# Kernel tuning notes

Hardware: AMD Instinct MI355X
Metric: run time of the kernel (lower is better)

## Reference

```python
import jax, jax.numpy as jnp
import numpy as np
import math

B, C, H, W = 16, 256, 96, 96
S = 3  # num_stages
OUT_C = 64


def _pos_encoding(c, h, w):
    # Faithful vectorization of generate_fixed_cosine_positional_encoding.
    pos_y = jnp.linspace(0.0, 1.0, h)
    pos_x = jnp.linspace(0.0, 1.0, w)
    py, px = jnp.meshgrid(pos_y, pos_x, indexing='ij')  # [H, W]
    i_vals = np.arange(0, c // 2, 2)                    # loop indices i
    freqs = jnp.exp(jnp.asarray(i_vals, jnp.float32) * -(math.log(10000.0) / (c // 2)))  # div_term[i//2]
    sin_part = jnp.sin(px[None] * freqs[:, None, None]) + jnp.sin(py[None] * freqs[:, None, None])
    cos_part = jnp.cos(px[None] * freqs[:, None, None]) + jnp.cos(py[None] * freqs[:, None, None])
    pe = jnp.zeros((c, h, w), jnp.float32)
    pe = pe.at[2 * i_vals].set(sin_part).at[2 * i_vals + 1].set(cos_part)
    return pe


def _nearest_resize(wmap, h, w):
    # torch F.interpolate(mode='nearest'): src_idx = floor(dst_idx * in/out)
    hw, ww = wmap.shape[-2], wmap.shape[-1]
    ih = (jnp.arange(h) * hw) // h
    iw = (jnp.arange(w) * ww) // w
    return wmap[..., ih[:, None], iw[None, :]]


def _conv1x1(x, w, b):
    return jnp.einsum('oc,bchw->bohw', w, x) + b[None, :, None, None]


def setup_inputs():
    key = jax.random.key(0)
    ks = jax.random.split(key, 12)
    sc = 0.3 / math.sqrt(C)
    return {
        'x1': jax.random.normal(ks[0], (B, C, H, W), jnp.float32),
        'x2': jax.random.normal(ks[1], (B, C, H, W), jnp.float32),
        'weight_vis': jax.random.uniform(ks[2], (B, H, W), jnp.float32),
        'weight_ir': jax.random.uniform(ks[3], (B, H, W), jnp.float32),
        'q_w': jax.random.normal(ks[4], (S, C, C), jnp.float32) * sc,
        'q_b': jnp.zeros((S, C), jnp.float32),
        'k_w': jax.random.normal(ks[5], (S, C, C), jnp.float32) * sc,
        'k_b': jnp.zeros((S, C), jnp.float32),
        'v_w': jax.random.normal(ks[6], (S, C, C), jnp.float32) * sc,
        'v_b': jnp.zeros((S, C), jnp.float32),
        'proj_w': jax.random.normal(ks[7], (OUT_C, C), jnp.float32) * sc,
        'proj_b': jnp.zeros((OUT_C,), jnp.float32),
    }


def reference(x1, x2, weight_vis, weight_ir, q_w, q_b, k_w, k_b, v_w, v_b, proj_w, proj_b):
    pe = _pos_encoding(x1.shape[1], x1.shape[2], x1.shape[3])  # combined_pos_encoding = pe1
    h, w = x1.shape[2], x1.shape[3]
    w_vis = _nearest_resize(weight_vis[:, None], h, w)  # [B,1,H,W]
    w_ir = _nearest_resize(weight_ir[:, None], h, w)
    fused = x1
    for i in range(S):
        x1 = x1 * w_vis
        x2 = x2 * w_ir
        q = _conv1x1(x1, q_w[i], q_b[i]) + pe[None]          # [B,C,H,W]
        k = _conv1x1(x2, k_w[i], k_b[i]) + pe[None]
        v = _conv1x1(x2, v_w[i], v_b[i])
        logits = jnp.einsum('bchw,bcgw->bchg', q, k)         # per-channel QK^T: [B,C,H,H]
        attn = jax.nn.softmax(logits, axis=-1)
        fused = jnp.einsum('bchg,bcgw->bchw', attn, v)       # [B,C,H,W]
        x1, x2 = fused, fused
    return _conv1x1(fused, proj_w, proj_b)                    # [B,64,H,W]
```

## Files before the change

kernel.cpp:

```cpp
#include <hip/hip_runtime.h>
#include <hip/hip_bf16.h>
#include <math.h>

#define NPOS 9216
#define PERB 2359296ull

typedef unsigned short u16;
typedef __attribute__((ext_vector_type(8))) short short8;
typedef __attribute__((ext_vector_type(4))) float f32x4;

__device__ inline u16 bfhi(float x) {
    unsigned int b = __float_as_uint(x);
    return (u16)((b + 0x7FFFu + ((b >> 16) & 1u)) >> 16);
}
__device__ inline float bf2f(u16 u) { return __uint_as_float(((unsigned int)u) << 16); }

typedef const __attribute__((address_space(1))) void* gvp;
typedef __attribute__((address_space(3))) void* lvp;
__device__ __forceinline__ void glds16(const void* g, void* l) {
    __builtin_amdgcn_global_load_lds((gvp)g, (lvp)l, 16, 0, 0);
}

__global__ __launch_bounds__(256) void tt_kernel(float* __restrict__ T)
{
    int idx = blockIdx.x * 256 + threadIdx.x;
    int c = idx / 96, p = idx - (idx / 96) * 96;
    int j = c >> 2, r = c & 3;
    float f = expf(-(float)(2 * j) * 0.07195578415f);
    float x = (float)p * (1.0f / 95.0f) * f;
    T[idx] = (r == 0) ? sinf(x) : (r == 1) ? cosf(x) : 0.0f;
}

__global__ __launch_bounds__(256) void wsplit(
    const float* __restrict__ qw, const float* __restrict__ kw,
    const float* __restrict__ vw, u16* __restrict__ whi, u16* __restrict__ wlo)
{
    int bid = blockIdx.x;
    int s = bid / 48, rem = bid % 48;
    int mat = rem / 16, rem2 = rem % 16;
    int mb = rem2 / 8, kb = rem2 % 8;
    const float* W = ((mat == 0) ? qw : (mat == 1) ? kw : vw) + (size_t)s * 65536;
    int t = threadIdx.x;
    int m = t >> 1, kh = (t & 1) * 16;
    const float* src = W + (size_t)(mb * 128 + m) * 256 + kb * 32 + kh;
    int s0 = kh >> 3;
    int sw = (m >> 1) & 3;
    size_t ob = (size_t)s * 196608 + (size_t)((mat * 2 + mb) * 8 + kb) * 4096
              + (size_t)m * 32;
    u16 hv[16], lv[16];
#pragma unroll
    for (int j = 0; j < 16; ++j) {
        float x = src[j];
        u16 h = bfhi(x);
        hv[j] = h;
        lv[j] = bfhi(x - bf2f(h));
    }
    *(uint4*)(whi + ob + ((s0 ^ sw) * 8))       = *(uint4*)hv;
    *(uint4*)(whi + ob + (((s0 + 1) ^ sw) * 8)) = *(uint4*)(hv + 8);
    *(uint4*)(wlo + ob + ((s0 ^ sw) * 8))       = *(uint4*)lv;
    *(uint4*)(wlo + ob + (((s0 + 1) ^ sw) * 8)) = *(uint4*)(lv + 8);
}

__global__ __launch_bounds__(512, 4) void gemm_qkv_mfma(
    const u16* __restrict__ whi, const u16* __restrict__ wlo,
    const float* __restrict__ srcq, const float* __restrict__ srckv,
    const float* __restrict__ qb, const float* __restrict__ kbias,
    const float* __restrict__ vb, const float* __restrict__ wvis,
    const float* __restrict__ wir, const float* __restrict__ Ttab,
    float* __restrict__ qo, float* __restrict__ ko, float* __restrict__ vo)
{
    __shared__ char LDSBUF[49152];
    u16* AH = (u16*)LDSBUF;
    u16* AL = AH + 8192;
    u16* BH = AL + 8192;
    u16* BL = BH + 4096;

    int t = threadIdx.x;
    int d = blockIdx.x + 3 * blockIdx.y;
    int role = (d & 7) * 27 + (d >> 3);
    int mat = role / 72, bn = role % 72;
    int b = blockIdx.z;

    const float* gB = ((mat == 0) ? srcq : srckv) + (size_t)b * PERB + bn * 128;
    const u16* gA0 = whi + (size_t)(mat * 2) * 32768;
    const u16* gA1 = wlo + (size_t)(mat * 2) * 32768;

    int wv = t >> 6;
    int wm = wv >> 1, wn = wv & 1;
    int rr = t & 15, gq = (t >> 4) & 3;

    int sxor = (gq ^ ((rr >> 1) & 3)) * 8;
    int offA0 = (wm * 64 + rr) * 32 + sxor;
    int offB0 = (wn * 64 + rr) * 32 + sxor;

    int arow = t >> 2, acol = (t & 3) * 8;
    size_t asrc0 = (size_t)arow * 32 + acol;
    size_t asrc1 = 32768 + (size_t)arow * 32 + acol;

    int bn_ = t & 127, bkh = t >> 7;
    int key = (bn_ >> 1) & 3;
    int wrB = bn_ * 32 + ((bkh ^ key) * 8);
    const float* bp = gB + (size_t)(bkh * 8) * NPOS + bn_;

    f32x4 acc[4][4];
#pragma unroll
    for (int i = 0; i < 4; ++i)
#pragma unroll
        for (int j = 0; j < 4; ++j) acc[i][j] = (f32x4){0.f, 0.f, 0.f, 0.f};

    float xv[8];
#pragma unroll
    for (int j = 0; j < 8; ++j) xv[j] = bp[(size_t)j * NPOS];

    for (int kq = 0; kq < 8; ++kq) {
        {
            glds16(gA0 + kq * 4096 + asrc0, &AH[t * 8]);
            glds16(gA0 + kq * 4096 + asrc1, &AH[t * 8 + 4096]);
            glds16(gA1 + kq * 4096 + asrc0, &AL[t * 8]);
            glds16(gA1 + kq * 4096 + asrc1, &AL[t * 8 + 4096]);
        }
        {
            u16 hv[8], lv[8];
#pragma unroll
            for (int j = 0; j < 8; ++j) {
                float x = xv[j];
                u16 h = bfhi(x);
                hv[j] = h;
                lv[j] = bfhi(x - bf2f(h));
            }
            *(uint4*)(&BH[wrB]) = *(uint4*)hv;
            *(uint4*)(&BL[wrB]) = *(uint4*)lv;
        }
        __syncthreads();

        if (kq < 7) {
#pragma unroll
            for (int j = 0; j < 8; ++j)
                xv[j] = bp[(size_t)((kq + 1) * 32 + j) * NPOS];
        }

        short8 bh[4], bl[4];
#pragma unroll
        for (int r = 0; r < 4; ++r) {
            bh[r] = *(const short8*)(&BH[offB0 + r * 512]);
            bl[r] = *(const short8*)(&BL[offB0 + r * 512]);
        }
#pragma unroll
        for (int f = 0; f < 4; ++f) {
            short8 ah = *(const short8*)(&AH[offA0 + f * 512]);
            short8 al = *(const short8*)(&AL[offA0 + f * 512]);
#pragma unroll
            for (int r = 0; r < 4; ++r) {
                acc[f][r] = __builtin_amdgcn_mfma_f32_16x16x32_bf16(ah, bh[r], acc[f][r], 0, 0, 0);
                acc[f][r] = __builtin_amdgcn_mfma_f32_16x16x32_bf16(ah, bl[r], acc[f][r], 0, 0, 0);
                acc[f][r] = __builtin_amdgcn_mfma_f32_16x16x32_bf16(al, bh[r], acc[f][r], 0, 0, 0);
            }
        }
        asm volatile("s_waitcnt lgkmcnt(0)" ::: "memory");
        __builtin_amdgcn_s_barrier();
        __builtin_amdgcn_sched_barrier(0);
    }

    float* SB = (float*)LDSBUF + (size_t)wv * (16 * 68);
    const float* wmap = ((mat == 0) ? wvis : wir) + (size_t)b * NPOS;
    const float* bias = (mat == 0) ? qb : (mat == 1) ? kbias : vb;
    float* outp = ((mat == 0) ? qo : (mat == 1) ? ko : vo) + (size_t)b * PERB;
    bool addpe = (mat != 2);

    int lane = t & 63;
    int lrow = lane >> 2;
    int lq   = lane & 3;
    int base_n = bn * 128 + wn * 64;

#pragma unroll
    for (int f = 0; f < 4; ++f) {
#pragma unroll
        for (int r = 0; r < 4; ++r)
#pragma unroll
            for (int ri = 0; ri < 4; ++ri)
                SB[(gq * 4 + ri) * 68 + (r * 16 + rr)] = acc[f][r][ri];
        int o = wm * 64 + f * 16 + lrow;
        float bo = bias[o];
        const float* tro = Ttab + o * 96;
        float* orow = outp + (size_t)o * NPOS;
#pragma unroll
        for (int qd = 0; qd < 4; ++qd) {
            int c0 = lq * 16 + qd * 4;
            int n = base_n + c0;
            float4 v4 = *(float4*)&SB[lrow * 68 + c0];
            float4 s4 = *(const float4*)&wmap[n];
            float4 o4;
            if (addpe) {
                int hh = n / 96, ww = n - hh * 96;
                float4 pw4 = *(const float4*)&tro[ww];
                float ph = tro[hh];
                o4.x = v4.x * s4.x + bo + pw4.x + ph;
                o4.y = v4.y * s4.y + bo + pw4.y + ph;
                o4.z = v4.z * s4.z + bo + pw4.z + ph;
                o4.w = v4.w * s4.w + bo + pw4.w + ph;
            } else {
                o4.x = v4.x * s4.x + bo;
                o4.y = v4.y * s4.y + bo;
                o4.z = v4.z * s4.z + bo;
                o4.w = v4.w * s4.w + bo;
            }
            *(float4*)&orow[n] = o4;
        }
    }
}

__global__ __launch_bounds__(192, 2) void attn_mfma(
    const float* __restrict__ q, const float* __restrict__ k,
    const float* __restrict__ v, float* __restrict__ fused)
{
    __shared__ char LB[76800];
    u16* QH = (u16*)LB;
    u16* QL = (u16*)(LB + 19200);
    u16* KH = (u16*)(LB + 38400);
    u16* KL = (u16*)(LB + 57600);
    float* OB = (float*)LB;

    int t = threadIdx.x;
    int bc = blockIdx.x;
    size_t base = (size_t)bc * NPOS;
    int wq = t >> 6, rr = t & 15, gq = (t >> 4) & 3;
    int sxor = (gq ^ ((rr >> 1) & 3)) * 8;

#pragma unroll
    for (int i = 0; i < 12; ++i) {
        int idx = i * 192 + t;
        int row = idx / 24, c4 = (idx % 24) * 4;
        int tile = c4 >> 5, kin = c4 & 31;
        int a = tile * 3072 + row * 32 + (((kin >> 3) ^ ((row >> 1) & 3)) << 3) + (kin & 7);
        float4 qv = *(const float4*)(q + base + row * 96 + c4);
        float4 kv = *(const float4*)(k + base + row * 96 + c4);
        unsigned int qh01, qh23, ql01, ql23, kh01, kh23, kl01, kl23;
        {
            u16 h0 = bfhi(qv.x), h1 = bfhi(qv.y), h2 = bfhi(qv.z), h3 = bfhi(qv.w);
            u16 l0 = bfhi(qv.x - bf2f(h0)), l1 = bfhi(qv.y - bf2f(h1));
            u16 l2 = bfhi(qv.z - bf2f(h2)), l3 = bfhi(qv.w - bf2f(h3));
            qh01 = (unsigned)h0 | ((unsigned)h1 << 16); qh23 = (unsigned)h2 | ((unsigned)h3 << 16);
            ql01 = (unsigned)l0 | ((unsigned)l1 << 16); ql23 = (unsigned)l2 | ((unsigned)l3 << 16);
        }
        {
            u16 h0 = bfhi(kv.x), h1 = bfhi(kv.y), h2 = bfhi(kv.z), h3 = bfhi(kv.w);
            u16 l0 = bfhi(kv.x - bf2f(h0)), l1 = bfhi(kv.y - bf2f(h1));
            u16 l2 = bfhi(kv.z - bf2f(h2)), l3 = bfhi(kv.w - bf2f(h3));
            kh01 = (unsigned)h0 | ((unsigned)h1 << 16); kh23 = (unsigned)h2 | ((unsigned)h3 << 16);
            kl01 = (unsigned)l0 | ((unsigned)l1 << 16); kl23 = (unsigned)l2 | ((unsigned)l3 << 16);
        }
        *(uint2*)(QH + a) = (uint2){qh01, qh23};
        *(uint2*)(QL + a) = (uint2){ql01, ql23};
        *(uint2*)(KH + a) = (uint2){kh01, kh23};
        *(uint2*)(KL + a) = (uint2){kl01, kl23};
    }
    __syncthreads();

    f32x4 acc[2][6];
#pragma unroll
    for (int mt = 0; mt < 2; ++mt)
#pragma unroll
        for (int nt = 0; nt < 6; ++nt) acc[mt][nt] = (f32x4){0.f, 0.f, 0.f, 0.f};

#pragma unroll
    for (int ks = 0; ks < 3; ++ks) {
        short8 qh2[2], ql2[2], kh6[6], kl6[6];
#pragma unroll
        for (int mt = 0; mt < 2; ++mt) {
            int ra = ks * 3072 + (wq * 32 + mt * 16 + rr) * 32 + sxor;
            qh2[mt] = *(const short8*)(QH + ra);
            ql2[mt] = *(const short8*)(QL + ra);
        }
#pragma unroll
        for (int nt = 0; nt < 6; ++nt) {
            int rb = ks * 3072 + (nt * 16 + rr) * 32 + sxor;
            kh6[nt] = *(const short8*)(KH + rb);
            kl6[nt] = *(const short8*)(KL + rb);
        }
#pragma unroll
        for (int mt = 0; mt < 2; ++mt)
#pragma unroll
            for (int nt = 0; nt < 6; ++nt) {
                acc[mt][nt] = __builtin_amdgcn_mfma_f32_16x16x32_bf16(qh2[mt], kh6[nt], acc[mt][nt], 0, 0, 0);
                acc[mt][nt] = __builtin_amdgcn_mfma_f32_16x16x32_bf16(qh2[mt], kl6[nt], acc[mt][nt], 0, 0, 0);
                acc[mt][nt] = __builtin_amdgcn_mfma_f32_16x16x32_bf16(ql2[mt], kh6[nt], acc[mt][nt], 0, 0, 0);
                acc[mt][nt] = __builtin_amdgcn_mfma_f32_16x16x32_bf16(ql2[mt], kl6[nt], acc[mt][nt], 0, 0, 0);
            }
    }

#pragma unroll
    for (int mt = 0; mt < 2; ++mt)
#pragma unroll
        for (int ri = 0; ri < 4; ++ri) {
            float mx = acc[mt][0][ri];
#pragma unroll
            for (int nt = 1; nt < 6; ++nt) mx = fmaxf(mx, acc[mt][nt][ri]);
            for (int dd = 1; dd < 16; dd <<= 1) mx = fmaxf(mx, __shfl_xor(mx, dd));
            float s = 0.0f;
#pragma unroll
            for (int nt = 0; nt < 6; ++nt) {
                float e = __expf(acc[mt][nt][ri] - mx);
                acc[mt][nt][ri] = e;
                s += e;
            }
            for (int dd = 1; dd < 16; dd <<= 1) s += __shfl_xor(s, dd);
            float inv = 1.0f / s;
#pragma unroll
            for (int nt = 0; nt < 6; ++nt) acc[mt][nt][ri] *= inv;
        }

    __syncthreads();

#pragma unroll
    for (int mt = 0; mt < 2; ++mt)
#pragma unroll
        for (int ri = 0; ri < 4; ++ri) {
            int row = wq * 32 + mt * 16 + gq * 4 + ri;
            int keyr = (row >> 1) & 3;
#pragma unroll
            for (int nt = 0; nt < 6; ++nt) {
                float val = acc[mt][nt][ri];
                u16 h = bfhi(val);
                u16 l = bfhi(val - bf2f(h));
                int slot = ((nt & 1) << 1) | (rr >> 3);
                int a = (nt >> 1) * 3072 + row * 32 + ((slot ^ keyr) << 3) + (rr & 7);
                QH[a] = h;
                QL[a] = l;
            }
        }
#pragma unroll
    for (int i = 0; i < 3; ++i) {
        int idx = i * 192 + t;
        int gq4 = idx / 24, wq4 = idx % 24;
        int g0 = gq4 * 4, w0 = wq4 * 4;
        float4 r0 = *(const float4*)(v + base + (size_t)(g0 + 0) * 96 + w0);
        float4 r1 = *(const float4*)(v + base + (size_t)(g0 + 1) * 96 + w0);
        float4 r2 = *(const float4*)(v + base + (size_t)(g0 + 2) * 96 + w0);
        float4 r3 = *(const float4*)(v + base + (size_t)(g0 + 3) * 96 + w0);
        int tile = g0 >> 5, kin = g0 & 31;
        int slot = kin >> 3, off = kin & 7;
#pragma unroll
        for (int j = 0; j < 4; ++j) {
            int w = w0 + j;
            float c0 = (j == 0) ? r0.x : (j == 1) ? r0.y : (j == 2) ? r0.z : r0.w;
            float c1 = (j == 0) ? r1.x : (j == 1) ? r1.y : (j == 2) ? r1.z : r1.w;
            float c2 = (j == 0) ? r2.x : (j == 1) ? r2.y : (j == 2) ? r2.z : r2.w;
            float c3 = (j == 0) ? r3.x : (j == 1) ? r3.y : (j == 2) ? r3.z : r3.w;
            u16 h0 = bfhi(c0), h1 = bfhi(c1), h2 = bfhi(c2), h3 = bfhi(c3);
            u16 l0 = bfhi(c0 - bf2f(h0)), l1 = bfhi(c1 - bf2f(h1));
            u16 l2 = bfhi(c2 - bf2f(h2)), l3 = bfhi(c3 - bf2f(h3));
            int a = tile * 3072 + w * 32 + ((slot ^ ((w >> 1) & 3)) << 3) + off;
            *(uint2*)(KH + a) = (uint2){(unsigned)h0 | ((unsigned)h1 << 16),
                                        (unsigned)h2 | ((unsigned)h3 << 16)};
            *(uint2*)(KL + a) = (uint2){(unsigned)l0 | ((unsigned)l1 << 16),
                                        (unsigned)l2 | ((unsigned)l3 << 16)};
        }
    }
    __syncthreads();

#pragma unroll
    for (int mt = 0; mt < 2; ++mt)
#pragma unroll
        for (int nt = 0; nt < 6; ++nt) acc[mt][nt] = (f32x4){0.f, 0.f, 0.f, 0.f};

#pragma unroll
    for (int ks = 0; ks < 3; ++ks) {
        short8 ph2[2], pl2[2], vh6[6], vl6[6];
#pragma unroll
        for (int mt = 0; mt < 2; ++mt) {
            int ra = ks * 3072 + (wq * 32 + mt * 16 + rr) * 32 + sxor;
            ph2[mt] = *(const short8*)(QH + ra);
            pl2[mt] = *(const short8*)(QL + ra);
        }
#pragma unroll
        for (int nt = 0; nt < 6; ++nt) {
            int rb = ks * 3072 + (nt * 16 + rr) * 32 + sxor;
            vh6[nt] = *(const short8*)(KH + rb);
            vl6[nt] = *(const short8*)(KL + rb);
        }
#pragma unroll
        for (int mt = 0; mt < 2; ++mt)
#pragma unroll
            for (int nt = 0; nt < 6; ++nt) {
                acc[mt][nt] = __builtin_amdgcn_mfma_f32_16x16x32_bf16(ph2[mt], vh6[nt], acc[mt][nt], 0, 0, 0);
                acc[mt][nt] = __builtin_amdgcn_mfma_f32_16x16x32_bf16(ph2[mt], vl6[nt], acc[mt][nt], 0, 0, 0);
                acc[mt][nt] = __builtin_amdgcn_mfma_f32_16x16x32_bf16(pl2[mt], vh6[nt], acc[mt][nt], 0, 0, 0);
            }
    }
    __syncthreads();

#pragma unroll
    for (int mt = 0; mt < 2; ++mt)
#pragma unroll
        for (int nt = 0; nt < 6; ++nt)
#pragma unroll
            for (int ri = 0; ri < 4; ++ri) {
                int row = wq * 32 + mt * 16 + gq * 4 + ri;
                OB[row * 100 + nt * 16 + rr] = acc[mt][nt][ri];
            }
    __syncthreads();
#pragma unroll
    for (int i = 0; i < 12; ++i) {
        int idx = i * 192 + t;
        int row = idx / 24, c4 = (idx % 24) * 4;
        float4 o = *(const float4*)&OB[row * 100 + c4];
        *(float4*)(fused + base + row * 96 + c4) = o;
    }
}

__global__ __launch_bounds__(256) void proj_kernel(
    const float* __restrict__ fused, const float* __restrict__ pw,
    const float* __restrict__ pb, float* __restrict__ out)
{
    __shared__ float As[16 * 68];
    __shared__ float Bs[16 * 128];

    int t  = threadIdx.x;
    int n0 = blockIdx.x * 128;
    int b  = blockIdx.y;
    const float* B = fused + (size_t)b * PERB;
    int tx = t & 15, ty = t >> 4;

    float acc[4][8];
#pragma unroll
    for (int i = 0; i < 4; ++i)
#pragma unroll
        for (int j = 0; j < 8; ++j) acc[i][j] = 0.0f;

    for (int k0 = 0; k0 < 256; k0 += 16) {
        {
            int m = t >> 2, c4 = (t & 3) * 4;
            float4 av = *(const float4*)(pw + (size_t)m * 256 + k0 + c4);
            As[(c4 + 0) * 68 + m] = av.x;
            As[(c4 + 1) * 68 + m] = av.y;
            As[(c4 + 2) * 68 + m] = av.z;
            As[(c4 + 3) * 68 + m] = av.w;
        }
#pragma unroll
        for (int l = 0; l < 2; ++l) {
            int f = t + l * 256;
            int c = f >> 5, n4 = (f & 31) * 4;
            *(float4*)(Bs + c * 128 + n4) =
                *(const float4*)(B + (size_t)(k0 + c) * NPOS + n0 + n4);
        }
        __syncthreads();
#pragma unroll
        for (int kk = 0; kk < 16; ++kk) {
            float a[4], bb[8];
            *(float4*)(&a[0])  = *(const float4*)(As + kk * 68 + ty * 4);
            *(float4*)(&bb[0]) = *(const float4*)(Bs + kk * 128 + tx * 8);
            *(float4*)(&bb[4]) = *(const float4*)(Bs + kk * 128 + tx * 8 + 4);
#pragma unroll
            for (int i = 0; i < 4; ++i)
#pragma unroll
                for (int j = 0; j < 8; ++j)
                    acc[i][j] = fmaf(a[i], bb[j], acc[i][j]);
        }
        __syncthreads();
    }

    int n = n0 + tx * 8;
#pragma unroll
    for (int i = 0; i < 4; ++i) {
        int o = ty * 4 + i;
        float bias = pb[o];
        float vals[8];
#pragma unroll
        for (int j = 0; j < 8; ++j) vals[j] = acc[i][j] + bias;
        float* op = out + ((size_t)b * 64 + o) * NPOS + n;
        *(float4*)(op)     = *(float4*)(&vals[0]);
        *(float4*)(op + 4) = *(float4*)(&vals[4]);
    }
}

extern "C" void kernel_launch(void* const* d_in, const int* in_sizes, int n_in,
                              void* d_out, int out_size, void* d_ws, size_t ws_size,
                              hipStream_t stream)
{
    const float* x1   = (const float*)d_in[0];
    const float* x2   = (const float*)d_in[1];
    const float* wvis = (const float*)d_in[2];
    const float* wir  = (const float*)d_in[3];
    const float* qw   = (const float*)d_in[4];
    const float* qb   = (const float*)d_in[5];
    const float* kw   = (const float*)d_in[6];
    const float* kb   = (const float*)d_in[7];
    const float* vw   = (const float*)d_in[8];
    const float* vb   = (const float*)d_in[9];
    const float* pw   = (const float*)d_in[10];
    const float* pb   = (const float*)d_in[11];
    float* out = (float*)d_out;

    float* ws = (float*)d_ws;
    size_t F = ws_size / 4;
    size_t fixed = 350000;
    size_t avail = (F > fixed) ? (F - fixed) : 0;
    int G = (int)(avail / (4 * PERB));
    if (G < 1) G = 1;
    if (G > 8) G = 8;

    float* ttab  = ws;
    float* qbuf  = ws + 24576;
    float* kbuf  = qbuf + (size_t)G * PERB;
    float* vbuf  = kbuf + (size_t)G * PERB;
    float* fbuf  = vbuf + (size_t)G * PERB;
    u16*   whiP  = (u16*)(fbuf + (size_t)G * PERB);
    u16*   wloP  = whiP + 589824;

    tt_kernel<<<dim3(96), 256, 0, stream>>>(ttab);
    wsplit<<<dim3(144), 256, 0, stream>>>(qw, kw, vw, whiP, wloP);

    for (int b0 = 0; b0 < 16; b0 += G) {
        int g = (16 - b0 < G) ? (16 - b0) : G;
        for (int s = 0; s < 3; ++s) {
            const float* sq  = (s == 0) ? (x1 + (size_t)b0 * PERB) : fbuf;
            const float* skv = (s == 0) ? (x2 + (size_t)b0 * PERB) : fbuf;
            gemm_qkv_mfma<<<dim3(3, 72, g), 512, 0, stream>>>(
                whiP + (size_t)s * 196608, wloP + (size_t)s * 196608,
                sq, skv,
                qb + (size_t)s * 256, kb + (size_t)s * 256, vb + (size_t)s * 256,
                wvis + (size_t)b0 * NPOS, wir + (size_t)b0 * NPOS,
                ttab, qbuf, kbuf, vbuf);
            attn_mfma<<<dim3(256 * g), 192, 0, stream>>>(qbuf, kbuf, vbuf, fbuf);
        }
        proj_kernel<<<dim3(72, g), 256, 0, stream>>>(
            fbuf, pw, pb, out + (size_t)b0 * 64 * NPOS);
    }
}
```

Before: 1.523 ms.

## Double-buffer weight tiles in LDS to overlap global loads with MFMA

The QKV GEMM now holds two LDS buffers for the split-bf16 weight tiles. While MFMAs consume one buffer, the next K-slice is fetched into the other with global_load_lds. The loop is unrolled by two, and explicit vmcnt/lgkmcnt waits plus barriers replace the single per-iteration sync. This aims to hide weight-load latency, but LDS use rises from 48KB to 80KB, which can cut the number of resident blocks per CU.

```diff
diff --git a/kernel.cpp b/kernel.cpp
--- a/kernel.cpp
+++ b/kernel.cpp
@@ -69,10 +69,10 @@
     const float* __restrict__ wir, const float* __restrict__ Ttab,
     float* __restrict__ qo, float* __restrict__ ko, float* __restrict__ vo)
 {
-    __shared__ char LDSBUF[49152];
-    u16* AH = (u16*)LDSBUF;
-    u16* AL = AH + 8192;
-    u16* BH = AL + 8192;
+    __shared__ char LDSBUF[81920];
+    u16* A0 = (u16*)LDSBUF;
+    u16* A1 = A0 + 16384;
+    u16* BH = A1 + 16384;
     u16* BL = BH + 4096;
 
     int t = threadIdx.x;
@@ -108,37 +108,31 @@
 #pragma unroll
         for (int j = 0; j < 4; ++j) acc[i][j] = (f32x4){0.f, 0.f, 0.f, 0.f};
 
+    auto STAGE_A = [&](int kk, u16* P) {
+        glds16(gA0 + kk * 4096 + asrc0, &P[t * 8]);
+        glds16(gA0 + kk * 4096 + asrc1, &P[t * 8 + 4096]);
+        glds16(gA1 + kk * 4096 + asrc0, &P[8192 + t * 8]);
+        glds16(gA1 + kk * 4096 + asrc1, &P[8192 + t * 8 + 4096]);
+    };
     float xv[8];
-#pragma unroll
-    for (int j = 0; j < 8; ++j) xv[j] = bp[(size_t)j * NPOS];
-
-    for (int kq = 0; kq < 8; ++kq) {
-        {
-            glds16(gA0 + kq * 4096 + asrc0, &AH[t * 8]);
-            glds16(gA0 + kq * 4096 + asrc1, &AH[t * 8 + 4096]);
-            glds16(gA1 + kq * 4096 + asrc0, &AL[t * 8]);
-            glds16(gA1 + kq * 4096 + asrc1, &AL[t * 8 + 4096]);
-        }
-        {
-            u16 hv[8], lv[8];
-#pragma unroll
-            for (int j = 0; j < 8; ++j) {
-                float x = xv[j];
-                u16 h = bfhi(x);
-                hv[j] = h;
-                lv[j] = bfhi(x - bf2f(h));
-            }
-            *(uint4*)(&BH[wrB]) = *(uint4*)hv;
-            *(uint4*)(&BL[wrB]) = *(uint4*)lv;
-        }
-        __syncthreads();
-
-        if (kq < 7) {
-#pragma unroll
-            for (int j = 0; j < 8; ++j)
-                xv[j] = bp[(size_t)((kq + 1) * 32 + j) * NPOS];
-        }
-
+    auto CONVB = [&]() {
+        u16 hv[8], lv[8];
+#pragma unroll
+        for (int j = 0; j < 8; ++j) {
+            float x = xv[j];
+            u16 h = bfhi(x);
+            hv[j] = h;
+            lv[j] = bfhi(x - bf2f(h));
+        }
+        *(uint4*)(&BH[wrB]) = *(uint4*)hv;
+        *(uint4*)(&BL[wrB]) = *(uint4*)lv;
+    };
+    auto LOADB = [&](int kk) {
+#pragma unroll
+        for (int j = 0; j < 8; ++j)
+            xv[j] = bp[(size_t)(kk * 32) * NPOS + (size_t)j * NPOS];
+    };
+    auto MFMA = [&](const u16* P) {
         short8 bh[4], bl[4];
 #pragma unroll
         for (int r = 0; r < 4; ++r) {
@@ -147,8 +141,8 @@
         }
 #pragma unroll
         for (int f = 0; f < 4; ++f) {
-            short8 ah = *(const short8*)(&AH[offA0 + f * 512]);
-            short8 al = *(const short8*)(&AL[offA0 + f * 512]);
+            short8 ah = *(const short8*)(&P[offA0 + f * 512]);
+            short8 al = *(const short8*)(&P[8192 + offA0 + f * 512]);
 #pragma unroll
             for (int r = 0; r < 4; ++r) {
                 acc[f][r] = __builtin_amdgcn_mfma_f32_16x16x32_bf16(ah, bh[r], acc[f][r], 0, 0, 0);
@@ -156,9 +150,35 @@
                 acc[f][r] = __builtin_amdgcn_mfma_f32_16x16x32_bf16(al, bh[r], acc[f][r], 0, 0, 0);
             }
         }
-        asm volatile("s_waitcnt lgkmcnt(0)" ::: "memory");
+    };
+
+    STAGE_A(0, A0);
+    LOADB(0);
+
+    for (int kq2 = 0; kq2 < 4; ++kq2) {
+        int kq = 2 * kq2;
+        STAGE_A(kq + 1, A1);
+        CONVB();
+        asm volatile("s_waitcnt vmcnt(4) lgkmcnt(0)" ::: "memory");
         __builtin_amdgcn_s_barrier();
-        __builtin_amdgcn_sched_barrier(0);
+        LOADB(kq + 1);
+        MFMA(A0);
+        __builtin_amdgcn_s_barrier();
+        if (kq2 < 3) {
+            STAGE_A(kq + 2, A0);
+            CONVB();
+            asm volatile("s_waitcnt vmcnt(4) lgkmcnt(0)" ::: "memory");
+            __builtin_amdgcn_s_barrier();
+            LOADB(kq + 2);
+            MFMA(A1);
+            __builtin_amdgcn_s_barrier();
+        } else {
+            CONVB();
+            asm volatile("s_waitcnt vmcnt(0) lgkmcnt(0)" ::: "memory");
+            __builtin_amdgcn_s_barrier();
+            MFMA(A1);
+            __builtin_amdgcn_s_barrier();
+        }
     }
 
     float* SB = (float*)LDSBUF + (size_t)wv * (16 * 68);
```

New measurement: 3.718 ms. +144.2%, slower.
